# Optimization experiments

Measured on AMD Instinct MI355X. Metric: run time of the kernel, lower is better.

Reference implementation:

```python
import jax, jax.numpy as jnp
import numpy as np

B, T, I, H, O = 32, 128, 256, 256, 128

def setup_inputs() -> dict:
    key = jax.random.key(0)
    k = jax.random.split(key, 7)
    init_k = 1.0 / np.sqrt(H)
    sentence = jax.random.normal(k[0], (B, T, I), dtype=jnp.float32)
    weight_lambda = jax.random.uniform(k[1], (H, H + I), minval=0.0, maxval=1.0, dtype=jnp.float32)
    weight_gamma = jax.random.uniform(k[2], (H, H + I), minval=-0.001 * init_k, maxval=0.001 * init_k, dtype=jnp.float32)
    weight = jax.random.uniform(k[3], (H, H + I), minval=-init_k, maxval=init_k, dtype=jnp.float32)
    bias = jax.random.uniform(k[4], (H,), minval=-init_k, maxval=init_k, dtype=jnp.float32)
    W_out = jax.random.uniform(k[5], (O, H), minval=-init_k, maxval=init_k, dtype=jnp.float32)
    b_out = jax.random.uniform(k[6], (O,), minval=-init_k, maxval=init_k, dtype=jnp.float32)
    return {"sentence": sentence, "weight_lambda": weight_lambda, "weight_gamma": weight_gamma,
            "weight": weight, "bias": bias, "W_out": W_out, "b_out": b_out}

def reference(sentence, weight_lambda, weight_gamma, weight, bias, W_out, b_out):
    b = sentence.shape[0]
    h0 = jnp.zeros((b, H), dtype=sentence.dtype)
    F0 = jnp.zeros((b, H, H + I), dtype=sentence.dtype)

    def step(carry, x_t):
        h, F = carry
        total_input = jnp.concatenate([x_t, h], axis=1)           # (B, I+H)
        total_weights = weight + F                                 # (B, H, I+H)
        h_new = jnp.tanh(jnp.einsum('bf,bhf->bh', total_input, total_weights) + bias)
        norm = jnp.linalg.norm(total_weights, axis=2, keepdims=True) + 1e-16  # (B, H, 1)
        h_new = h_new / norm[..., 0]
        F_new = weight_lambda * (F / norm) + weight_gamma * jnp.einsum('bf,bh->bhf', total_input, h_new)
        return (h_new, F_new), None

    (h_T, F_T), _ = jax.lax.scan(step, (h0, F0), jnp.swapaxes(sentence, 0, 1))
    tag_space = h_T @ W_out.T + b_out
    return tag_space, h_T, F_T
```

## Files before the change

kernel.cpp:

```cpp
#include <hip/hip_runtime.h>

#define BB 32
#define TT 128
#define II 256
#define HH 256
#define OO 128
#define FWID 512


typedef unsigned long long u64;
typedef float f32x2 __attribute__((ext_vector_type(2)));

__device__ __forceinline__ f32x2 mk2(float a, float b) { f32x2 r; r.x = a; r.y = b; return r; }

__device__ __forceinline__ f32x2 pk_fma(f32x2 a, f32x2 b, f32x2 c) {
    f32x2 d;
    asm("v_pk_fma_f32 %0, %1, %2, %3" : "=v"(d) : "v"(a), "v"(b), "v"(c));
    return d;
}
__device__ __forceinline__ f32x2 pk_mul(f32x2 a, f32x2 b) {
    f32x2 d;
    asm("v_pk_mul_f32 %0, %1, %2" : "=v"(d) : "v"(a), "v"(b));
    return d;
}
__device__ __forceinline__ f32x2 pk_add(f32x2 a, f32x2 b) {
    f32x2 d;
    asm("v_pk_add_f32 %0, %1, %2" : "=v"(d) : "v"(a), "v"(b));
    return d;
}

template<int CTRL>
__device__ __forceinline__ float dpp_add(float x) {
    int t = __builtin_amdgcn_update_dpp(0, __float_as_int(x), CTRL, 0xF, 0xF, true);
    return x + __int_as_float(t);
}
__device__ __forceinline__ float row16_sum(float x) {
    x = dpp_add<0x128>(x);
    x = dpp_add<0x124>(x);
    x = dpp_add<0x122>(x);
    x = dpp_add<0x121>(x);
    return x;
}

__device__ __forceinline__ u64 slot_ld(const u64* p) {
    return __hip_atomic_load(p, __ATOMIC_RELAXED, __HIP_MEMORY_SCOPE_AGENT);
}

__device__ __forceinline__ void gather_to_lds(const u64* base, int lane, unsigned us,
                                              float* dst, int* flag, int fval) {
    const u64* p = base + 4 * lane;
    u64 a, b, c, d;
    for (;;) {
        a = slot_ld(p);
        b = slot_ld(p + 1);
        c = slot_ld(p + 2);
        d = slot_ld(p + 3);
        bool ok = ((unsigned)(a >> 32) >= us) & ((unsigned)(b >> 32) >= us) &
                  ((unsigned)(c >> 32) >= us) & ((unsigned)(d >> 32) >= us);
        if (__all(ok)) break;
    }
    float4 hv;
    hv.x = __uint_as_float((unsigned)a);
    hv.y = __uint_as_float((unsigned)b);
    hv.z = __uint_as_float((unsigned)c);
    hv.w = __uint_as_float((unsigned)d);
    *reinterpret_cast<float4*>(dst + 4 * lane) = hv;
    if (lane == 0)
        __hip_atomic_store(flag, fval, __ATOMIC_RELEASE, __HIP_MEMORY_SCOPE_WORKGROUP);
}

__global__ __launch_bounds__(512, 2)
void stpn_kernel(const float* __restrict__ x,
                 const float* __restrict__ wlam,
                 const float* __restrict__ wgam,
                 const float* __restrict__ w,
                 const float* __restrict__ bias,
                 const float* __restrict__ wout,
                 const float* __restrict__ bout,
                 float* __restrict__ out,
                 u64* __restrict__ slots)
{
    __shared__ __align__(16) float lh[2][HH];
    __shared__ int lflag[2];

    const int tid  = threadIdx.x;
    const int bk   = blockIdx.x;
    const int b    = bk & 31;
    const int sl   = bk >> 5;
    const int wv   = tid >> 6;
    const int lane = tid & 63;
    const int g    = tid >> 4;
    const int i    = tid & 15;
    const int r    = sl * 32 + (g & 31);

    if (tid < 2) lflag[tid] = 0;

    f32x2 W2[16], Lm2[16], G2[16], F2[16];
    {
        const float4* wr = reinterpret_cast<const float4*>(w    + (size_t)r * FWID);
        const float4* lr = reinterpret_cast<const float4*>(wlam + (size_t)r * FWID);
        const float4* gr = reinterpret_cast<const float4*>(wgam + (size_t)r * FWID);
#pragma unroll
        for (int k = 0; k < 8; ++k) {
            float4 t;
            t = wr[k * 16 + i]; W2[2*k]  = mk2(t.x, t.y); W2[2*k+1]  = mk2(t.z, t.w);
            t = lr[k * 16 + i]; Lm2[2*k] = mk2(t.x, t.y); Lm2[2*k+1] = mk2(t.z, t.w);
            t = gr[k * 16 + i]; G2[2*k]  = mk2(t.x, t.y); G2[2*k+1]  = mk2(t.z, t.w);
            F2[2*k] = mk2(0.f, 0.f); F2[2*k+1] = mk2(0.f, 0.f);
        }
    }
    const float bj = bias[r];
    float hl = 0.f;

    float4 px0, px1, px2, px3;
    {
        const float4* xb4 = reinterpret_cast<const float4*>(x + (size_t)b * TT * II);
        px0 = xb4[i]; px1 = xb4[16 + i]; px2 = xb4[32 + i]; px3 = xb4[48 + i];
    }

    __syncthreads();

    for (int s = 0; s < TT; ++s) {
        const int par = s & 1;

        f32x2 X2[8];
        X2[0] = mk2(px0.x, px0.y); X2[1] = mk2(px0.z, px0.w);
        X2[2] = mk2(px1.x, px1.y); X2[3] = mk2(px1.z, px1.w);
        X2[4] = mk2(px2.x, px2.y); X2[5] = mk2(px2.z, px2.w);
        X2[6] = mk2(px3.x, px3.y); X2[7] = mk2(px3.z, px3.w);

        f32x2 tw2[8];
        f32x2 dx2 = mk2(0.f, 0.f), nv2 = mk2(0.f, 0.f);
#pragma unroll
        for (int j = 0; j < 8; ++j) {
            f32x2 t = pk_add(W2[j], F2[j]);
            dx2 = pk_fma(X2[j], t, dx2);
            nv2 = pk_fma(t, t, nv2);
        }
#pragma unroll
        for (int j = 0; j < 8; ++j) {
            tw2[j] = pk_add(W2[8 + j], F2[8 + j]);
            nv2 = pk_fma(tw2[j], tw2[j], nv2);
        }
        float dxs = dx2.x + dx2.y;
        float nrm = nv2.x + nv2.y;
        dxs = row16_sum(dxs);
        nrm = row16_sum(nrm);
        const float invn = __builtin_amdgcn_rsqf(nrm);
        const f32x2 invn2 = mk2(invn, invn);
        const float dxb = dxs + bj;

#pragma unroll
        for (int j = 0; j < 16; ++j) F2[j] = pk_mul(Lm2[j], pk_mul(F2[j], invn2));

        if (wv == 0) {
            gather_to_lds(slots + ((size_t)par * BB + b) * HH, lane,
                          (unsigned)s, lh[par], &lflag[par], s + 1);
        }

        while (__hip_atomic_load(&lflag[par], __ATOMIC_ACQUIRE, __HIP_MEMORY_SCOPE_WORKGROUP) <= s) {}
        const float4* lh4 = reinterpret_cast<const float4*>(lh[par]);
        float4 ha = lh4[i], hb = lh4[16 + i], hc = lh4[32 + i], hd = lh4[48 + i];
        f32x2 H2[8];
        H2[0] = mk2(ha.x, ha.y); H2[1] = mk2(ha.z, ha.w);
        H2[2] = mk2(hb.x, hb.y); H2[3] = mk2(hb.z, hb.w);
        H2[4] = mk2(hc.x, hc.y); H2[5] = mk2(hc.z, hc.w);
        H2[6] = mk2(hd.x, hd.y); H2[7] = mk2(hd.z, hd.w);

        f32x2 a2 = pk_mul(H2[0], tw2[0]);
        f32x2 b2 = pk_mul(H2[1], tw2[1]);
        a2 = pk_fma(H2[2], tw2[2], a2);
        b2 = pk_fma(H2[3], tw2[3], b2);
        a2 = pk_fma(H2[4], tw2[4], a2);
        b2 = pk_fma(H2[5], tw2[5], b2);
        a2 = pk_fma(H2[6], tw2[6], a2);
        b2 = pk_fma(H2[7], tw2[7], b2);
        f32x2 c2 = pk_add(a2, b2);
        float dh = c2.x + c2.y;
        dh = row16_sum(dh);

        const float e = __expf(2.0f * (dxb + dh));
        const float h = (1.0f - 2.0f * __builtin_amdgcn_rcpf(e + 1.0f)) * invn;
        hl = h;

        if (i == 0) {
            __hip_atomic_store(slots + ((size_t)(par ^ 1) * BB + b) * HH + r,
                               ((u64)(unsigned)(s + 1) << 32) | (unsigned)__float_as_uint(h),
                               __ATOMIC_RELAXED, __HIP_MEMORY_SCOPE_AGENT);
        }

        if (s + 1 < TT) {
            const float4* xn = reinterpret_cast<const float4*>(x + ((size_t)b * TT + (s + 1)) * II);
            px0 = xn[i]; px1 = xn[16 + i]; px2 = xn[32 + i]; px3 = xn[48 + i];
        }

        const f32x2 h2v = mk2(h, h);
#pragma unroll
        for (int j = 0; j < 8; ++j)
            F2[j] = pk_fma(pk_mul(X2[j], G2[j]), h2v, F2[j]);
#pragma unroll
        for (int j = 0; j < 8; ++j)
            F2[8 + j] = pk_fma(pk_mul(G2[8 + j], H2[j]), h2v, F2[8 + j]);
    }

    {
        float4* fo = reinterpret_cast<float4*>(out + 12288 + ((size_t)b * HH + r) * FWID);
#pragma unroll
        for (int k = 0; k < 8; ++k) {
            float4 v;
            v.x = F2[2*k].x; v.y = F2[2*k].y; v.z = F2[2*k+1].x; v.w = F2[2*k+1].y;
            fo[k * 16 + i] = v;
        }
    }
    if (i == 0) out[4096 + (size_t)b * HH + r] = hl;

    if (sl == 0) {
        if (wv == 0) {
            gather_to_lds(slots + ((size_t)(TT & 1) * BB + b) * HH, lane,
                          (unsigned)TT, lh[0], &lflag[0], TT + 1);
        }
        while (__hip_atomic_load(&lflag[0], __ATOMIC_ACQUIRE, __HIP_MEMORY_SCOPE_WORKGROUP) <= TT) {}
        if (tid < OO) {
            const float* hv = lh[0];
            float acc = bout[tid];
            const float* wo = wout + (size_t)tid * HH;
#pragma unroll 4
            for (int jj = 0; jj < HH; ++jj) acc = fmaf(wo[jj], hv[jj], acc);
            out[(size_t)b * OO + tid] = acc;
        }
    }
}

extern "C" void kernel_launch(void* const* d_in, const int* in_sizes, int n_in,
                              void* d_out, int out_size, void* d_ws, size_t ws_size,
                              hipStream_t stream) {
    (void)in_sizes; (void)n_in; (void)out_size; (void)ws_size;
    const float* x    = (const float*)d_in[0];
    const float* wlam = (const float*)d_in[1];
    const float* wgam = (const float*)d_in[2];
    const float* w    = (const float*)d_in[3];
    const float* bias = (const float*)d_in[4];
    const float* wout = (const float*)d_in[5];
    const float* bout = (const float*)d_in[6];
    float* out = (float*)d_out;

    u64* slots = (u64*)d_ws;

    hipMemsetAsync(d_ws, 0, 2ull * BB * HH * 8ull, stream);

    void* args[] = {(void*)&x, (void*)&wlam, (void*)&wgam, (void*)&w, (void*)&bias,
                    (void*)&wout, (void*)&bout, (void*)&out, (void*)&slots};
    hipLaunchCooperativeKernel((void*)stpn_kernel, dim3(256), dim3(512), args, 0, stream);
}
```

Before: 265.8 us.

## Process two batch elements per block sharing weight registers, 32-lane row groups

Each block now handles two batch rows (b and b+16) for 16 hidden rows instead of one batch row for 32 hidden rows. Each 32-lane group holds a quarter of a weight row, so W, lambda and gamma registers are shared across both batch elements. Reductions now span 32 lanes via DPP plus a ds_swizzle step, and the two batch chains are interleaved within each timestep so one chain's work can cover the other's wait on the cross-block exchange. The cooperative launch is replaced by a plain launch, which drops the co-residency guarantee that the spin-wait exchange between blocks depends on.

```diff
diff --git a/kernel.cpp b/kernel.cpp
--- a/kernel.cpp
+++ b/kernel.cpp
@@ -34,12 +34,20 @@
     int t = __builtin_amdgcn_update_dpp(0, __float_as_int(x), CTRL, 0xF, 0xF, true);
     return x + __int_as_float(t);
 }
-__device__ __forceinline__ float row16_sum(float x) {
-    x = dpp_add<0x128>(x);
-    x = dpp_add<0x124>(x);
-    x = dpp_add<0x122>(x);
-    x = dpp_add<0x121>(x);
-    return x;
+__device__ __forceinline__ void red32_pair(float& a, float& b) {
+    a = dpp_add<0x128>(a); b = dpp_add<0x128>(b);
+    a = dpp_add<0x124>(a); b = dpp_add<0x124>(b);
+    a = dpp_add<0x122>(a); b = dpp_add<0x122>(b);
+    a = dpp_add<0x121>(a); b = dpp_add<0x121>(b);
+    int ta = __builtin_amdgcn_ds_swizzle(__float_as_int(a), 0x401F);
+    int tb = __builtin_amdgcn_ds_swizzle(__float_as_int(b), 0x401F);
+    a += __int_as_float(ta); b += __int_as_float(tb);
+}
+__device__ __forceinline__ float red32(float a) {
+    a = dpp_add<0x128>(a); a = dpp_add<0x124>(a);
+    a = dpp_add<0x122>(a); a = dpp_add<0x121>(a);
+    a += __int_as_float(__builtin_amdgcn_ds_swizzle(__float_as_int(a), 0x401F));
+    return a;
 }
 
 __device__ __forceinline__ u64 slot_ld(const u64* p) {
@@ -80,42 +88,51 @@
                  float* __restrict__ out,
                  u64* __restrict__ slots)
 {
-    __shared__ __align__(16) float lh[2][HH];
-    __shared__ int lflag[2];
+    __shared__ __align__(16) float lh[2][2][HH];
+    __shared__ int lflag[4];
 
     const int tid  = threadIdx.x;
     const int bk   = blockIdx.x;
-    const int b    = bk & 31;
-    const int sl   = bk >> 5;
+    const int p    = bk & 15;
+    const int sl   = bk >> 4;
+    const int bA   = p;
+    const int bB   = p + 16;
     const int wv   = tid >> 6;
     const int lane = tid & 63;
-    const int g    = tid >> 4;
-    const int i    = tid & 15;
-    const int r    = sl * 32 + (g & 31);
-
-    if (tid < 2) lflag[tid] = 0;
-
-    f32x2 W2[16], Lm2[16], G2[16], F2[16];
+    const int g    = tid >> 5;
+    const int i    = tid & 31;
+    const int r    = sl * 16 + g;
+
+    if (tid < 4) lflag[tid] = 0;
+
+    f32x2 W2[8], Lm2[8], G2[8], FA[8], FB[8];
     {
         const float4* wr = reinterpret_cast<const float4*>(w    + (size_t)r * FWID);
         const float4* lr = reinterpret_cast<const float4*>(wlam + (size_t)r * FWID);
         const float4* gr = reinterpret_cast<const float4*>(wgam + (size_t)r * FWID);
 #pragma unroll
-        for (int k = 0; k < 8; ++k) {
+        for (int k = 0; k < 4; ++k) {
             float4 t;
-            t = wr[k * 16 + i]; W2[2*k]  = mk2(t.x, t.y); W2[2*k+1]  = mk2(t.z, t.w);
-            t = lr[k * 16 + i]; Lm2[2*k] = mk2(t.x, t.y); Lm2[2*k+1] = mk2(t.z, t.w);
-            t = gr[k * 16 + i]; G2[2*k]  = mk2(t.x, t.y); G2[2*k+1]  = mk2(t.z, t.w);
-            F2[2*k] = mk2(0.f, 0.f); F2[2*k+1] = mk2(0.f, 0.f);
+            t = wr[k * 32 + i]; W2[2*k]  = mk2(t.x, t.y); W2[2*k+1]  = mk2(t.z, t.w);
+            t = lr[k * 32 + i]; Lm2[2*k] = mk2(t.x, t.y); Lm2[2*k+1] = mk2(t.z, t.w);
+            t = gr[k * 32 + i]; G2[2*k]  = mk2(t.x, t.y); G2[2*k+1]  = mk2(t.z, t.w);
+            FA[2*k] = mk2(0.f, 0.f); FA[2*k+1] = mk2(0.f, 0.f);
+            FB[2*k] = mk2(0.f, 0.f); FB[2*k+1] = mk2(0.f, 0.f);
         }
     }
     const float bj = bias[r];
-    float hl = 0.f;
-
-    float4 px0, px1, px2, px3;
+    float hlA = 0.f, hlB = 0.f;
+
+    f32x2 XA[4], XB[4];
     {
-        const float4* xb4 = reinterpret_cast<const float4*>(x + (size_t)b * TT * II);
-        px0 = xb4[i]; px1 = xb4[16 + i]; px2 = xb4[32 + i]; px3 = xb4[48 + i];
+        const float4* xa4 = reinterpret_cast<const float4*>(x + (size_t)bA * TT * II);
+        const float4* xb4 = reinterpret_cast<const float4*>(x + (size_t)bB * TT * II);
+        float4 t0 = xa4[i], t1 = xa4[32 + i];
+        XA[0] = mk2(t0.x, t0.y); XA[1] = mk2(t0.z, t0.w);
+        XA[2] = mk2(t1.x, t1.y); XA[3] = mk2(t1.z, t1.w);
+        t0 = xb4[i]; t1 = xb4[32 + i];
+        XB[0] = mk2(t0.x, t0.y); XB[1] = mk2(t0.z, t0.w);
+        XB[2] = mk2(t1.x, t1.y); XB[3] = mk2(t1.z, t1.w);
     }
 
     __syncthreads();
@@ -123,110 +140,194 @@
     for (int s = 0; s < TT; ++s) {
         const int par = s & 1;
 
-        f32x2 X2[8];
-        X2[0] = mk2(px0.x, px0.y); X2[1] = mk2(px0.z, px0.w);
-        X2[2] = mk2(px1.x, px1.y); X2[3] = mk2(px1.z, px1.w);
-        X2[4] = mk2(px2.x, px2.y); X2[5] = mk2(px2.z, px2.w);
-        X2[6] = mk2(px3.x, px3.y); X2[7] = mk2(px3.z, px3.w);
-
-        f32x2 tw2[8];
-        f32x2 dx2 = mk2(0.f, 0.f), nv2 = mk2(0.f, 0.f);
-#pragma unroll
-        for (int j = 0; j < 8; ++j) {
-            f32x2 t = pk_add(W2[j], F2[j]);
-            dx2 = pk_fma(X2[j], t, dx2);
-            nv2 = pk_fma(t, t, nv2);
-        }
-#pragma unroll
-        for (int j = 0; j < 8; ++j) {
-            tw2[j] = pk_add(W2[8 + j], F2[8 + j]);
-            nv2 = pk_fma(tw2[j], tw2[j], nv2);
-        }
-        float dxs = dx2.x + dx2.y;
-        float nrm = nv2.x + nv2.y;
-        dxs = row16_sum(dxs);
-        nrm = row16_sum(nrm);
-        const float invn = __builtin_amdgcn_rsqf(nrm);
-        const f32x2 invn2 = mk2(invn, invn);
-        const float dxb = dxs + bj;
-
-#pragma unroll
-        for (int j = 0; j < 16; ++j) F2[j] = pk_mul(Lm2[j], pk_mul(F2[j], invn2));
-
-        if (wv == 0) {
-            gather_to_lds(slots + ((size_t)par * BB + b) * HH, lane,
-                          (unsigned)s, lh[par], &lflag[par], s + 1);
-        }
-
-        while (__hip_atomic_load(&lflag[par], __ATOMIC_ACQUIRE, __HIP_MEMORY_SCOPE_WORKGROUP) <= s) {}
-        const float4* lh4 = reinterpret_cast<const float4*>(lh[par]);
-        float4 ha = lh4[i], hb = lh4[16 + i], hc = lh4[32 + i], hd = lh4[48 + i];
-        f32x2 H2[8];
-        H2[0] = mk2(ha.x, ha.y); H2[1] = mk2(ha.z, ha.w);
-        H2[2] = mk2(hb.x, hb.y); H2[3] = mk2(hb.z, hb.w);
-        H2[4] = mk2(hc.x, hc.y); H2[5] = mk2(hc.z, hc.w);
-        H2[6] = mk2(hd.x, hd.y); H2[7] = mk2(hd.z, hd.w);
-
-        f32x2 a2 = pk_mul(H2[0], tw2[0]);
-        f32x2 b2 = pk_mul(H2[1], tw2[1]);
-        a2 = pk_fma(H2[2], tw2[2], a2);
-        b2 = pk_fma(H2[3], tw2[3], b2);
-        a2 = pk_fma(H2[4], tw2[4], a2);
-        b2 = pk_fma(H2[5], tw2[5], b2);
-        a2 = pk_fma(H2[6], tw2[6], a2);
-        b2 = pk_fma(H2[7], tw2[7], b2);
-        f32x2 c2 = pk_add(a2, b2);
-        float dh = c2.x + c2.y;
-        dh = row16_sum(dh);
-
-        const float e = __expf(2.0f * (dxb + dh));
-        const float h = (1.0f - 2.0f * __builtin_amdgcn_rcpf(e + 1.0f)) * invn;
-        hl = h;
-
-        if (i == 0) {
-            __hip_atomic_store(slots + ((size_t)(par ^ 1) * BB + b) * HH + r,
-                               ((u64)(unsigned)(s + 1) << 32) | (unsigned)__float_as_uint(h),
-                               __ATOMIC_RELAXED, __HIP_MEMORY_SCOPE_AGENT);
-        }
-
-        if (s + 1 < TT) {
-            const float4* xn = reinterpret_cast<const float4*>(x + ((size_t)b * TT + (s + 1)) * II);
-            px0 = xn[i]; px1 = xn[16 + i]; px2 = xn[32 + i]; px3 = xn[48 + i];
-        }
-
-        const f32x2 h2v = mk2(h, h);
-#pragma unroll
-        for (int j = 0; j < 8; ++j)
-            F2[j] = pk_fma(pk_mul(X2[j], G2[j]), h2v, F2[j]);
-#pragma unroll
-        for (int j = 0; j < 8; ++j)
-            F2[8 + j] = pk_fma(pk_mul(G2[8 + j], H2[j]), h2v, F2[8 + j]);
+        {
+            f32x2 tw[4];
+            f32x2 dx2 = mk2(0.f, 0.f), nv2 = mk2(0.f, 0.f);
+#pragma unroll
+            for (int j = 0; j < 4; ++j) {
+                f32x2 t = pk_add(W2[j], FA[j]);
+                dx2 = pk_fma(XA[j], t, dx2);
+                nv2 = pk_fma(t, t, nv2);
+            }
+#pragma unroll
+            for (int j = 0; j < 4; ++j) {
+                tw[j] = pk_add(W2[4 + j], FA[4 + j]);
+                nv2 = pk_fma(tw[j], tw[j], nv2);
+            }
+            float dxs = dx2.x + dx2.y;
+            float nrm = nv2.x + nv2.y;
+            red32_pair(dxs, nrm);
+            const float invn = __builtin_amdgcn_rsqf(nrm);
+            const f32x2 invn2 = mk2(invn, invn);
+            const float dxb = dxs + bj;
+#pragma unroll
+            for (int j = 0; j < 8; ++j) FA[j] = pk_mul(Lm2[j], pk_mul(FA[j], invn2));
+
+            if (wv == 0) {
+                gather_to_lds(slots + ((size_t)par * BB + bA) * HH, lane,
+                              (unsigned)s, lh[par][0], &lflag[par * 2 + 0], s + 1);
+            }
+            while (__hip_atomic_load(&lflag[par * 2 + 0], __ATOMIC_ACQUIRE,
+                                     __HIP_MEMORY_SCOPE_WORKGROUP) <= s) {}
+            const float4* lh4 = reinterpret_cast<const float4*>(lh[par][0]);
+            float4 h0 = lh4[i], h1 = lh4[32 + i];
+            f32x2 H2[4];
+            H2[0] = mk2(h0.x, h0.y); H2[1] = mk2(h0.z, h0.w);
+            H2[2] = mk2(h1.x, h1.y); H2[3] = mk2(h1.z, h1.w);
+
+            f32x2 a2 = pk_mul(H2[0], tw[0]);
+            f32x2 b2 = pk_mul(H2[1], tw[1]);
+            a2 = pk_fma(H2[2], tw[2], a2);
+            b2 = pk_fma(H2[3], tw[3], b2);
+            f32x2 c2 = pk_add(a2, b2);
+            float dh = red32(c2.x + c2.y);
+
+            const float e = __expf(2.0f * (dxb + dh));
+            const float h = (1.0f - 2.0f * __builtin_amdgcn_rcpf(e + 1.0f)) * invn;
+            hlA = h;
+
+            if (i == 0) {
+                __hip_atomic_store(slots + ((size_t)(par ^ 1) * BB + bA) * HH + r,
+                                   ((u64)(unsigned)(s + 1) << 32) | (unsigned)__float_as_uint(h),
+                                   __ATOMIC_RELAXED, __HIP_MEMORY_SCOPE_AGENT);
+            }
+
+            float4 t0n, t1n;
+            const bool pf = (s + 1 < TT);
+            if (pf) {
+                const float4* xn = reinterpret_cast<const float4*>(x + ((size_t)bA * TT + (s + 1)) * II);
+                t0n = xn[i]; t1n = xn[32 + i];
+            }
+            const f32x2 h2v = mk2(h, h);
+#pragma unroll
+            for (int j = 0; j < 4; ++j)
+                FA[j] = pk_fma(pk_mul(XA[j], G2[j]), h2v, FA[j]);
+#pragma unroll
+            for (int j = 0; j < 4; ++j)
+                FA[4 + j] = pk_fma(pk_mul(G2[4 + j], H2[j]), h2v, FA[4 + j]);
+            if (pf) {
+                XA[0] = mk2(t0n.x, t0n.y); XA[1] = mk2(t0n.z, t0n.w);
+                XA[2] = mk2(t1n.x, t1n.y); XA[3] = mk2(t1n.z, t1n.w);
+            }
+        }
+
+        {
+            f32x2 tw[4];
+            f32x2 dx2 = mk2(0.f, 0.f), nv2 = mk2(0.f, 0.f);
+#pragma unroll
+            for (int j = 0; j < 4; ++j) {
+                f32x2 t = pk_add(W2[j], FB[j]);
+                dx2 = pk_fma(XB[j], t, dx2);
+                nv2 = pk_fma(t, t, nv2);
+            }
+#pragma unroll
+            for (int j = 0; j < 4; ++j) {
+                tw[j] = pk_add(W2[4 + j], FB[4 + j]);
+                nv2 = pk_fma(tw[j], tw[j], nv2);
+            }
+            float dxs = dx2.x + dx2.y;
+            float nrm = nv2.x + nv2.y;
+            red32_pair(dxs, nrm);
+            const float invn = __builtin_amdgcn_rsqf(nrm);
+            const f32x2 invn2 = mk2(invn, invn);
+            const float dxb = dxs + bj;
+#pragma unroll
+            for (int j = 0; j < 8; ++j) FB[j] = pk_mul(Lm2[j], pk_mul(FB[j], invn2));
+
+            if (wv == 1) {
+                gather_to_lds(slots + ((size_t)par * BB + bB) * HH, lane,
+                              (unsigned)s, lh[par][1], &lflag[par * 2 + 1], s + 1);
+            }
+            while (__hip_atomic_load(&lflag[par * 2 + 1], __ATOMIC_ACQUIRE,
+                                     __HIP_MEMORY_SCOPE_WORKGROUP) <= s) {}
+            const float4* lh4 = reinterpret_cast<const float4*>(lh[par][1]);
+            float4 h0 = lh4[i], h1 = lh4[32 + i];
+            f32x2 H2[4];
+            H2[0] = mk2(h0.x, h0.y); H2[1] = mk2(h0.z, h0.w);
+            H2[2] = mk2(h1.x, h1.y); H2[3] = mk2(h1.z, h1.w);
+
+            f32x2 a2 = pk_mul(H2[0], tw[0]);
+            f32x2 b2 = pk_mul(H2[1], tw[1]);
+            a2 = pk_fma(H2[2], tw[2], a2);
+            b2 = pk_fma(H2[3], tw[3], b2);
+            f32x2 c2 = pk_add(a2, b2);
+            float dh = red32(c2.x + c2.y);
+
+            const float e = __expf(2.0f * (dxb + dh));
+            const float h = (1.0f - 2.0f * __builtin_amdgcn_rcpf(e + 1.0f)) * invn;
+            hlB = h;
+
+            if (i == 0) {
+                __hip_atomic_store(slots + ((size_t)(par ^ 1) * BB + bB) * HH + r,
+                                   ((u64)(unsigned)(s + 1) << 32) | (unsigned)__float_as_uint(h),
+                                   __ATOMIC_RELAXED, __HIP_MEMORY_SCOPE_AGENT);
+            }
+
+            float4 t0n, t1n;
+            const bool pf = (s + 1 < TT);
+            if (pf) {
+                const float4* xn = reinterpret_cast<const float4*>(x + ((size_t)bB * TT + (s + 1)) * II);
+                t0n = xn[i]; t1n = xn[32 + i];
+            }
+            const f32x2 h2v = mk2(h, h);
+#pragma unroll
+            for (int j = 0; j < 4; ++j)
+                FB[j] = pk_fma(pk_mul(XB[j], G2[j]), h2v, FB[j]);
+#pragma unroll
+            for (int j = 0; j < 4; ++j)
+                FB[4 + j] = pk_fma(pk_mul(G2[4 + j], H2[j]), h2v, FB[4 + j]);
+            if (pf) {
+                XB[0] = mk2(t0n.x, t0n.y); XB[1] = mk2(t0n.z, t0n.w);
+                XB[2] = mk2(t1n.x, t1n.y); XB[3] = mk2(t1n.z, t1n.w);
+            }
+        }
     }
 
     {
-        float4* fo = reinterpret_cast<float4*>(out + 12288 + ((size_t)b * HH + r) * FWID);
-#pragma unroll
-        for (int k = 0; k < 8; ++k) {
+        float4* foA = reinterpret_cast<float4*>(out + 12288 + ((size_t)bA * HH + r) * FWID);
+        float4* foB = reinterpret_cast<float4*>(out + 12288 + ((size_t)bB * HH + r) * FWID);
+#pragma unroll
+        for (int k = 0; k < 4; ++k) {
             float4 v;
-            v.x = F2[2*k].x; v.y = F2[2*k].y; v.z = F2[2*k+1].x; v.w = F2[2*k+1].y;
-            fo[k * 16 + i] = v;
-        }
-    }
-    if (i == 0) out[4096 + (size_t)b * HH + r] = hl;
+            v.x = FA[2*k].x; v.y = FA[2*k].y; v.z = FA[2*k+1].x; v.w = FA[2*k+1].y;
+            foA[k * 32 + i] = v;
+            v.x = FB[2*k].x; v.y = FB[2*k].y; v.z = FB[2*k+1].x; v.w = FB[2*k+1].y;
+            foB[k * 32 + i] = v;
+        }
+    }
+    if (i == 0) {
+        out[4096 + (size_t)bA * HH + r] = hlA;
+        out[4096 + (size_t)bB * HH + r] = hlB;
+    }
 
     if (sl == 0) {
         if (wv == 0) {
-            gather_to_lds(slots + ((size_t)(TT & 1) * BB + b) * HH, lane,
-                          (unsigned)TT, lh[0], &lflag[0], TT + 1);
-        }
-        while (__hip_atomic_load(&lflag[0], __ATOMIC_ACQUIRE, __HIP_MEMORY_SCOPE_WORKGROUP) <= TT) {}
+            gather_to_lds(slots + ((size_t)(TT & 1) * BB + bA) * HH, lane,
+                          (unsigned)TT, lh[0][0], &lflag[0], TT + 1);
+        }
+        if (wv == 1) {
+            gather_to_lds(slots + ((size_t)(TT & 1) * BB + bB) * HH, lane,
+                          (unsigned)TT, lh[0][1], &lflag[1], TT + 1);
+        }
         if (tid < OO) {
-            const float* hv = lh[0];
+            while (__hip_atomic_load(&lflag[0], __ATOMIC_ACQUIRE,
+                                     __HIP_MEMORY_SCOPE_WORKGROUP) <= TT) {}
+            const float* hv = lh[0][0];
             float acc = bout[tid];
             const float* wo = wout + (size_t)tid * HH;
 #pragma unroll 4
             for (int jj = 0; jj < HH; ++jj) acc = fmaf(wo[jj], hv[jj], acc);
-            out[(size_t)b * OO + tid] = acc;
+            out[(size_t)bA * OO + tid] = acc;
+        } else if (tid < 2 * OO) {
+            const int o = tid - OO;
+            while (__hip_atomic_load(&lflag[1], __ATOMIC_ACQUIRE,
+                                     __HIP_MEMORY_SCOPE_WORKGROUP) <= TT) {}
+            const float* hv = lh[0][1];
+            float acc = bout[o];
+            const float* wo = wout + (size_t)o * HH;
+#pragma unroll 4
+            for (int jj = 0; jj < HH; ++jj) acc = fmaf(wo[jj], hv[jj], acc);
+            out[(size_t)bB * OO + o] = acc;
         }
     }
 }
@@ -248,7 +349,6 @@
 
     hipMemsetAsync(d_ws, 0, 2ull * BB * HH * 8ull, stream);
 
-    void* args[] = {(void*)&x, (void*)&wlam, (void*)&wgam, (void*)&w, (void*)&bias,
-                    (void*)&wout, (void*)&bout, (void*)&out, (void*)&slots};
-    hipLaunchCooperativeKernel((void*)stpn_kernel, dim3(256), dim3(512), args, 0, stream);
-}
+    hipLaunchKernelGGL(stpn_kernel, dim3(256), dim3(512), 0, stream,
+                       x, wlam, wgam, w, bias, wout, bout, out, slots);
+}
```

After: 329.7 us. 24.0% more time.
